# Performance work log

Hardware: AMD Instinct MI355X
Metric: run time of the kernel (lower is better)

The kernel has to match this reference:

```python
import jax, jax.numpy as jnp
import numpy as np

B, N = 1, 6
C, H, W = 256, 32, 88          # featureShape
ORH, ORW = 256, 704            # transformed image shape
OC = 128                       # out_channels
DV = jnp.arange(1.0, 45.0, 1.0)  # depth bin centers, d_conf=(1,45,1)
D = DV.shape[0]                # 44
BN_EPS = 1e-3


def _conv(x, w, b, pad):
    y = jax.lax.conv_general_dilated(x, w, (1, 1), [(pad, pad), (pad, pad)],
                                     dimension_numbers=("NCHW", "OIHW", "NCHW"))
    return y + b[None, :, None, None]


def _bn(x, g, be, m, v):
    scale = g / jnp.sqrt(v + BN_EPS)
    return (x - m[None, :, None, None]) * scale[None, :, None, None] + be[None, :, None, None]


def _frustum():
    ds = jnp.broadcast_to(DV[:, None, None], (D, H, W))
    xs = jnp.broadcast_to(jnp.linspace(0.0, ORW - 1.0, W)[None, None, :], (D, H, W))
    ys = jnp.broadcast_to(jnp.linspace(0.0, ORH - 1.0, H)[None, :, None], (D, H, W))
    return jnp.stack((xs, ys, ds), -1)  # (D,H,W,3)


def _forward(rot, trans, K, prot, ptrans, feats,
             w1, b1, g1, be1, m1, v1, w2, b2, g2, be2, m2, v2, w3, b3):
    # ---- geometry: undo image augmentation, unproject, map cam->ego ----
    fr = _frustum()
    pts = fr[None, None] - ptrans[:, :, None, None, None, :]              # (B,N,D,H,W,3)
    pts = jnp.einsum("bnij,bndhwj->bndhwi", jnp.linalg.inv(prot), pts)
    pts = jnp.concatenate((pts[..., :2] * pts[..., 2:3], pts[..., 2:3]), -1)
    combine = jnp.einsum("bnij,bnjk->bnik", rot, jnp.linalg.inv(K))
    geom = jnp.einsum("bnij,bndhwj->bndhwi", combine, pts) + trans[:, :, None, None, None, :]
    # ---- depth net (conv-bn-relu x2 + 1x1 head) ----
    x = feats.reshape(B * N, C, H, W)
    x = jax.nn.relu(_bn(_conv(x, w1, b1, 1), g1, be1, m1, v1))
    x = jax.nn.relu(_bn(_conv(x, w2, b2, 1), g2, be2, m2, v2))
    x = _conv(x, w3, b3, 0)                                              # (BN, OC+2, H, W)
    mu, log_sigma, f = x[:, 0], x[:, 1], x[:, 2:]
    sigma = jnp.exp(log_sigma) + 1e-6
    # per-pixel Gaussian over depth bins, normalized over D
    gauss = jnp.exp(-0.5 * (DV[None, :, None, None] - mu[:, None]) ** 2 / (sigma[:, None] ** 2))  # (BN,D,H,W)
    gauss = gauss / (gauss.sum(1, keepdims=True) + 1e-6)
    # outer product depth-dist x features -> (BN, OC, D, H, W)
    out = gauss[:, None] * f[:, :, None]
    out = out.reshape(B, N, OC, D, H, W).transpose(0, 1, 3, 4, 5, 2)     # (B,N,D,H,W,OC)
    return geom, out


def setup_inputs():
    key = jax.random.key(0)
    ks = jax.random.split(key, 9)
    eye = jnp.eye(3)
    rot = eye + 0.1 * jax.random.normal(ks[0], (B, N, 3, 3), jnp.float32)
    trans = jax.random.normal(ks[1], (B, N, 3), jnp.float32)
    Kbase = jnp.array([[600.0, 0.0, 352.0], [0.0, 600.0, 128.0], [0.0, 0.0, 1.0]])
    K = jnp.broadcast_to(Kbase, (B, N, 3, 3)) * (1.0 + 0.01 * jax.random.normal(ks[2], (B, N, 3, 3)))
    prot = eye + 0.05 * jax.random.normal(ks[3], (B, N, 3, 3), jnp.float32)
    ptrans = jax.random.normal(ks[4], (B, N, 3), jnp.float32)
    feats = 0.5 * jax.random.normal(ks[5], (B, N, C, H, W), jnp.float32)
    w1 = 0.02 * jax.random.normal(ks[6], (C, C, 3, 3), jnp.float32); b1 = jnp.zeros((C,))
    w2 = 0.02 * jax.random.normal(ks[7], (C, C, 3, 3), jnp.float32); b2 = jnp.zeros((C,))
    w3 = 0.02 * jax.random.normal(ks[8], (OC + 2, C, 1, 1), jnp.float32); b3 = jnp.zeros((OC + 2,))
    ones = jnp.ones((C,)); zeros = jnp.zeros((C,))
    return dict(cam2ego_rot=rot, cam2ego_trans=trans, cam_intrins=K,
                post_cam2ego_rot=prot, post_cam2ego_trans=ptrans, img_feats=feats,
                w1=w1, b1=b1, g1=ones, be1=zeros, m1=zeros, v1=ones,
                w2=w2, b2=b2, g2=ones, be2=zeros, m2=zeros, v2=ones,
                w3=w3, b3=b3)


def reference(cam2ego_rot, cam2ego_trans, cam_intrins, post_cam2ego_rot, post_cam2ego_trans, img_feats,
              w1, b1, g1, be1, m1, v1, w2, b2, g2, be2, m2, v2, w3, b3):
    return _forward(cam2ego_rot, cam2ego_trans, cam_intrins, post_cam2ego_rot, post_cam2ego_trans, img_feats,
                    w1, b1, g1, be1, m1, v1, w2, b2, g2, be2, m2, v2, w3, b3)
```

## Files before the change

kernel.cpp:

```cpp
#include <hip/hip_runtime.h>
#include <hip/hip_fp16.h>
#include <hip/hip_fp8.h>
#include <stdint.h>

typedef _Float16 f16;
typedef _Float16 half8 __attribute__((ext_vector_type(8)));
typedef _Float16 half4v __attribute__((ext_vector_type(4)));
typedef float floatx4 __attribute__((ext_vector_type(4)));
typedef long long i64;
typedef long long i64x2 __attribute__((ext_vector_type(2)));

#define NCAM 6
#define NPIX 16896
#define CIN 256
#define OUT1_OFF 2230272

#define AB_OFF     4096
#define W3P_OFF    16384
#define W1P_OFF    163840
#define W2P_OFF    1343488
#define XPAD_OFF   2523136
#define Y1P_OFF    11923456
#define XPAD8_BYTES 4700160
#define Y1P8_OFF   (XPAD_OFF + XPAD8_BYTES)
#define Y3_WS_OFF  21323776
#define Y3_BYTES   8921088

#define PIPE_BAR6()  asm volatile("s_waitcnt vmcnt(6) lgkmcnt(0)\n\ts_barrier" ::: "memory")
#define PIPE_BAR0()  asm volatile("s_waitcnt vmcnt(0) lgkmcnt(0)\n\ts_barrier" ::: "memory")
#define PIPE_BARL()  asm volatile("s_waitcnt lgkmcnt(0)\n\ts_barrier" ::: "memory")

__device__ __forceinline__ void gld16(const void* gsrc, void* ldst) {
    typedef __attribute__((address_space(1))) const uint32_t GBuf;
    typedef __attribute__((address_space(3))) uint32_t LBuf;
    __builtin_amdgcn_global_load_lds((GBuf*)(uintptr_t)gsrc,
                                     (LBuf*)(uint32_t)(uintptr_t)ldst,
                                     16, 0, 0);
}

__device__ __forceinline__ uint8_t f2fp8(float v) {
    __hip_fp8_e4m3 q(v);
    return (uint8_t)q.__x;
}

__device__ __forceinline__ int fp8pos(int c) {
    int c128 = c & 127;
    int P  = c128 >> 6;
    int kh = (c128 >> 5) & 1;
    int ks = (c128 >> 3) & 3;
    return (c >> 7) * 128 + (P * 4 + ks) * 16 + kh * 8 + (c & 7);
}

__device__ __forceinline__ void inv3(const float* m, float* o) {
    float a=m[0],b=m[1],c=m[2],d=m[3],e=m[4],f=m[5],g=m[6],h=m[7],i=m[8];
    float A  =  (e*i - f*h);
    float Bc = -(d*i - f*g);
    float Cc =  (d*h - e*g);
    float det = a*A + b*Bc + c*Cc;
    float r = 1.0f/det;
    o[0]=A*r;   o[1]=-(b*i - c*h)*r; o[2]= (b*f - c*e)*r;
    o[3]=Bc*r;  o[4]= (a*i - c*g)*r; o[5]=-(a*f - c*d)*r;
    o[6]=Cc*r;  o[7]=-(a*h - b*g)*r; o[8]= (a*e - b*d)*r;
}

__device__ __forceinline__ void geom_point(int idx,
        const float* __restrict__ rot, const float* __restrict__ trans,
        const float* __restrict__ K, const float* __restrict__ prot,
        const float* __restrict__ ptrans, float* __restrict__ out) {
    int w = idx % 88;
    int h = (idx / 88) % 32;
    int d = (idx / 2816) % 44;
    int n = idx / 123904;
    float P[9], Km[9], R[9], iP[9], iK[9], C[9];
    #pragma unroll
    for (int i = 0; i < 9; ++i) { P[i]=prot[n*9+i]; Km[i]=K[n*9+i]; R[i]=rot[n*9+i]; }
    inv3(P, iP);
    inv3(Km, iK);
    #pragma unroll
    for (int i = 0; i < 3; ++i)
        #pragma unroll
        for (int j = 0; j < 3; ++j)
            C[i*3+j] = R[i*3+0]*iK[0*3+j] + R[i*3+1]*iK[1*3+j] + R[i*3+2]*iK[2*3+j];
    float fx = w * (703.0f / 87.0f);
    float fy = h * (255.0f / 31.0f);
    float fz = d + 1.0f;
    float px = fx - ptrans[n*3+0], py = fy - ptrans[n*3+1], pz = fz - ptrans[n*3+2];
    float q0 = iP[0]*px + iP[1]*py + iP[2]*pz;
    float q1 = iP[3]*px + iP[4]*py + iP[5]*pz;
    float q2 = iP[6]*px + iP[7]*py + iP[8]*pz;
    float r0 = q0 * q2, r1 = q1 * q2, r2 = q2;
    out[idx*3 + 0] = C[0]*r0 + C[1]*r1 + C[2]*r2 + trans[n*3+0];
    out[idx*3 + 1] = C[3]*r0 + C[4]*r1 + C[5]*r2 + trans[n*3+1];
    out[idx*3 + 2] = C[6]*r0 + C[7]*r1 + C[8]*r2 + trans[n*3+2];
}

__global__ __launch_bounds__(256) void fused_prep(
        const float* __restrict__ rot, const float* __restrict__ trans,
        const float* __restrict__ K, const float* __restrict__ prot,
        const float* __restrict__ ptrans, const float* __restrict__ feats,
        const float* __restrict__ w1, const float* __restrict__ w2,
        const float* __restrict__ w3,
        const float* __restrict__ b1, const float* __restrict__ g1,
        const float* __restrict__ be1, const float* __restrict__ m1, const float* __restrict__ v1,
        const float* __restrict__ b2, const float* __restrict__ g2,
        const float* __restrict__ be2, const float* __restrict__ m2, const float* __restrict__ v2,
        const float* __restrict__ b3,
        uint8_t* __restrict__ w1p, uint8_t* __restrict__ w2p, f16* __restrict__ w3p,
        float* __restrict__ ab, uint8_t* __restrict__ xpad8, uint8_t* __restrict__ y1p8,
        float* __restrict__ geomOut) {
    int bid = blockIdx.x;
    int t = threadIdx.x;
    if (bid < 12) {
        uint8_t* buf = (bid < 6) ? xpad8 : y1p8;
        int n = bid % 6;
        for (int i = t; i < 3904; i += 256) {
            int u = i >> 4, c = i & 15;
            int h, w;
            if (u < 90)       { h = 0;       w = u; }
            else if (u < 180) { h = 33;      w = u - 90; }
            else if (u < 212) { h = u - 179; w = 0; }
            else              { h = u - 211; w = 89; }
            *(uint4*)&buf[((size_t)((n*34 + h)*90 + w))*256 + c*16] = uint4{0,0,0,0};
        }
        return;
    }
    if (bid < 716) {
        int oc = bid - 12;
        if (oc < 512) {
            const float* s = ((oc < 256) ? w1 : w2) + (size_t)(oc & 255) * 2304;
            uint8_t* dst = ((oc < 256) ? w1p : w2p) + (size_t)(oc & 255) * 2304;
            for (int idx = t; idx < 2304; idx += 256) {
                int win = idx >> 7, b = idx & 127;
                int sl = b >> 4, j = b & 15;
                int P = sl >> 2, ks = sl & 3, kh = j >> 3, jj = j & 7;
                int kwin = (2*P + kh)*32 + ks*8 + jj;
                int Kg = win*128 + kwin;
                int tap = Kg >> 8, c = Kg & 255;
                dst[idx] = f2fp8(s[c*9 + tap] * 16.0f);
            }
        } else {
            int r = oc - 512;
            w3p[r * 256 + t] = (r < 130) ? (f16)w3[r * 256 + t] : (f16)0.0f;
        }
        return;
    }
    if (bid < 1484) {
        __shared__ float tile[64][89];
        int b = bid - 716;
        int n = b >> 7;
        int h = (b >> 2) & 31;
        int icg = b & 3;
        int ic0 = icg * 64;
        #pragma unroll
        for (int j = 0; j < 22; ++j) {
            int idx = j * 256 + t;
            int r = idx / 88, w = idx - r * 88;
            tile[r][w] = feats[((size_t)(n*256 + ic0 + r) * 32 + h) * 88 + w];
        }
        __syncthreads();
        for (int j = 0; j < 6; ++j) {
            int idx = j * 256 + t;
            if (idx < 1408) {
                int w = idx >> 4, cq = idx & 15;
                int c = cq * 4;
                int ca = ic0 + c;
                uint32_t u = (uint32_t)f2fp8(tile[c][w])
                           | ((uint32_t)f2fp8(tile[c+1][w]) << 8)
                           | ((uint32_t)f2fp8(tile[c+2][w]) << 16)
                           | ((uint32_t)f2fp8(tile[c+3][w]) << 24);
                size_t px = (size_t)((n*34 + h + 1) * 90 + (w + 1));
                *(uint32_t*)&xpad8[px*256 + fp8pos(ca)] = u;
            }
        }
        return;
    }
    if (bid == 1484) {
        float a1 = g1[t] * rsqrtf(v1[t] + 1e-3f);
        ab[t]       = a1 * 0.0625f;
        ab[256 + t] = (b1[t] - m1[t]) * a1 + be1[t];
        float a2 = g2[t] * rsqrtf(v2[t] + 1e-3f);
        ab[512 + t] = a2 * 0.0625f;
        ab[768 + t] = (b2[t] - m2[t]) * a2 + be2[t];
        if (t < 192) ab[1024 + t] = (t < 130) ? b3[t] : 0.0f;
        return;
    }
    int idx = (bid - 1485) * 256 + t;
    geom_point(idx, rot, trans, K, prot, ptrans, geomOut);
}

__global__ void geom_k(const float* __restrict__ rot, const float* __restrict__ trans,
                       const float* __restrict__ K, const float* __restrict__ prot,
                       const float* __restrict__ ptrans, float* __restrict__ out) {
    int idx = blockIdx.x * 256 + threadIdx.x;
    geom_point(idx, rot, trans, K, prot, ptrans, out);
}

template<bool FP8OUT>
__global__ __launch_bounds__(256, 3) void conv8_mfma(
        const uint8_t* __restrict__ xin,
        const uint8_t* __restrict__ wp,
        const float* __restrict__ ab, int abOff,
        uint8_t* __restrict__ yout8,
        f16* __restrict__ yout16)
{
    __shared__ alignas(16) uint8_t Ald[2][64 * 128];
    __shared__ alignas(16) uint8_t Bld[2][128 * 128];
    int t = threadIdx.x;
    int l = t & 63;
    int wid = t >> 6;
    int bid = (blockIdx.x & 7) * 66 + (blockIdx.x >> 3);
    int bm = bid & 3;
    int bn = bid >> 2;
    int p0 = bn * 128;
    int wm = wid >> 1, wn = wid & 1;
    int swz = (l & 7) ^ (l >> 3);

    const uint8_t* asrc = wp + (size_t)(bm*64 + wid*16 + (l >> 3)) * 2304 + swz * 16;
    size_t bsrc[4];
    #pragma unroll
    for (int i = 0; i < 4; ++i) {
        int p = p0 + wid*32 + i*8 + (l >> 3);
        int n = p / 2816; int rem = p - n * 2816;
        int hh = rem / 88; int ww = rem - hh * 88;
        bsrc[i] = (size_t)((n*34 + hh) * 90 + ww) * 256 + swz * 16;
    }
    int aoff = wid * 2048 + l * 16;
    int boff = wid * 4096 + l * 16;

    floatx4 acc[2][4] = {};

    auto stage = [&](int win, uint8_t* Ab, uint8_t* Bb) {
        int tap = win >> 1;
        int koff = ((tap/3) * 90 + (tap%3)) * 256 + (win & 1) * 128;
        const uint8_t* aw = asrc + win * 128;
        gld16(aw,             Ab + aoff);
        gld16(aw + 8 * 2304,  Ab + aoff + 1024);
        #pragma unroll
        for (int j = 0; j < 4; ++j)
            gld16(xin + bsrc[j] + koff, Bb + boff + j * 1024);
    };
    auto compute = [&](const uint8_t* Ab, const uint8_t* Bb) {
        #pragma unroll
        for (int P = 0; P < 2; ++P) {
            i64x2 af[2], bf[4];
            int sl = (((P << 2) | (l >> 4)) ^ (l & 7)) * 16;
            #pragma unroll
            for (int m = 0; m < 2; ++m) {
                int row = wm*32 + m*16 + (l & 15);
                af[m] = *(const i64x2*)&Ab[row * 128 + sl];
            }
            #pragma unroll
            for (int n = 0; n < 4; ++n) {
                int row = wn*64 + n*16 + (l & 15);
                bf[n] = *(const i64x2*)&Bb[row * 128 + sl];
            }
            __builtin_amdgcn_s_setprio(1);
            #pragma unroll
            for (int m = 0; m < 2; ++m)
                #pragma unroll
                for (int n = 0; n < 4; ++n) {
                    acc[m][n] = __builtin_amdgcn_mfma_f32_16x16x32_fp8_fp8(af[m].x, bf[n].x, acc[m][n], 0, 0, 0);
                    acc[m][n] = __builtin_amdgcn_mfma_f32_16x16x32_fp8_fp8(af[m].y, bf[n].y, acc[m][n], 0, 0, 0);
                }
            __builtin_amdgcn_s_setprio(0);
        }
    };

    stage(0, Ald[0], Bld[0]);
    stage(1, Ald[1], Bld[1]);
    #pragma unroll 1
    for (int win = 0; win < 16; win += 2) {
        PIPE_BAR6(); compute(Ald[0], Bld[0]);
        PIPE_BARL(); stage(win + 2, Ald[0], Bld[0]);
        PIPE_BAR6(); compute(Ald[1], Bld[1]);
        PIPE_BARL(); stage(win + 3, Ald[1], Bld[1]);
    }
    PIPE_BAR6(); compute(Ald[0], Bld[0]);
    PIPE_BAR0(); compute(Ald[1], Bld[1]);

    int ocb = bm*64 + wm*32;
    #pragma unroll
    for (int m = 0; m < 2; ++m) {
        int oc0 = ocb + m*16 + (l >> 4) * 4;
        float4 av = *(const float4*)&ab[abOff + oc0];
        float4 bv = *(const float4*)&ab[abOff + 256 + oc0];
        #pragma unroll
        for (int n = 0; n < 4; ++n) {
            int p = p0 + wn*64 + n*16 + (l & 15);
            int ni = p / 2816; int rem = p - ni * 2816;
            int hh = rem / 88; int ww = rem - hh * 88;
            size_t pxb = (size_t)((ni*34 + hh + 1) * 90 + (ww + 1)) * 256;
            float v0 = fmaxf(fmaf(acc[m][n][0], av.x, bv.x), 0.0f);
            float v1 = fmaxf(fmaf(acc[m][n][1], av.y, bv.y), 0.0f);
            float v2 = fmaxf(fmaf(acc[m][n][2], av.z, bv.z), 0.0f);
            float v3 = fmaxf(fmaf(acc[m][n][3], av.w, bv.w), 0.0f);
            if (FP8OUT) {
                uint32_t u = (uint32_t)f2fp8(v0)
                           | ((uint32_t)f2fp8(v1) << 8)
                           | ((uint32_t)f2fp8(v2) << 16)
                           | ((uint32_t)f2fp8(v3) << 24);
                *(uint32_t*)&yout8[pxb + fp8pos(oc0)] = u;
            } else {
                half4v hv;
                hv[0] = (f16)v0; hv[1] = (f16)v1; hv[2] = (f16)v2; hv[3] = (f16)v3;
                *(half4v*)&yout16[pxb + oc0] = hv;
            }
        }
    }
}

__global__ __launch_bounds__(256) void conv3_mfma(
        const f16* __restrict__ xin,
        const f16* __restrict__ wp3,
        const float* __restrict__ b3p,
        float* __restrict__ y3)
{
    __shared__ alignas(16) f16 Ald[3][64 * 64];
    __shared__ alignas(16) f16 Bld[3][128 * 64];
    int t = threadIdx.x;
    int l = t & 63;
    int wid = t >> 6;
    int bm = blockIdx.x % 3;
    int bn = blockIdx.x / 3;
    int p0 = bn * 128;
    int wm = wid >> 1, wn = wid & 1;
    int swz = (l & 7) ^ (l >> 3);

    const f16* asrc = wp3 + (size_t)(bm*64 + wid*16 + (l >> 3)) * 256 + swz * 8;
    size_t bsrc[4];
    #pragma unroll
    for (int i = 0; i < 4; ++i) {
        int p = p0 + wid*32 + i*8 + (l >> 3);
        int n = p / 2816; int rem = p - n * 2816;
        int hh = rem / 88; int ww = rem - hh * 88;
        bsrc[i] = (size_t)((n*34 + hh) * 90 + ww) * 256 + swz * 8;
    }
    int aoff = wid * 16 * 64;
    int boff = wid * 32 * 64;

    floatx4 acc[2][4] = {};

    auto stage = [&](int kt, f16* Ab, f16* Bb) {
        int koff = (1 * 90 + 1) * 256 + kt * 64;
        int k0 = kt * 64;
        gld16(asrc + k0,            Ab + aoff);
        gld16(asrc + k0 + 8 * 256,  Ab + aoff + 8 * 64);
        gld16(xin + bsrc[0] + koff, Bb + boff);
        gld16(xin + bsrc[1] + koff, Bb + boff + 8 * 64);
        gld16(xin + bsrc[2] + koff, Bb + boff + 16 * 64);
        gld16(xin + bsrc[3] + koff, Bb + boff + 24 * 64);
    };
    auto compute = [&](const f16* Ab, const f16* Bb) {
        #pragma unroll
        for (int kk = 0; kk < 2; ++kk) {
            half8 af[2], bf[4];
            int kslot = kk * 4 + (l >> 4);
            #pragma unroll
            for (int m = 0; m < 2; ++m) {
                int row = wm*32 + m*16 + (l & 15);
                af[m] = *(const half8*)&Ab[row * 64 + ((kslot ^ (row & 7)) * 8)];
            }
            #pragma unroll
            for (int n = 0; n < 4; ++n) {
                int row = wn*64 + n*16 + (l & 15);
                bf[n] = *(const half8*)&Bb[row * 64 + ((kslot ^ (row & 7)) * 8)];
            }
            __builtin_amdgcn_s_setprio(1);
            #pragma unroll
            for (int m = 0; m < 2; ++m)
                #pragma unroll
                for (int n = 0; n < 4; ++n)
                    acc[m][n] = __builtin_amdgcn_mfma_f32_16x16x32_f16(af[m], bf[n], acc[m][n], 0, 0, 0);
            __builtin_amdgcn_s_setprio(0);
        }
    };

    stage(0, Ald[0], Bld[0]);
    stage(1, Ald[1], Bld[1]);
    PIPE_BAR6(); stage(2, Ald[2], Bld[2]); compute(Ald[0], Bld[0]);
    PIPE_BAR6(); stage(3, Ald[0], Bld[0]); compute(Ald[1], Bld[1]);
    PIPE_BAR6(); compute(Ald[2], Bld[2]);
    PIPE_BAR0(); compute(Ald[0], Bld[0]);

    int ocb = bm*64 + wm*32;
    #pragma unroll
    for (int m = 0; m < 2; ++m) {
        int oc0 = ocb + m*16 + (l >> 4) * 4;
        if (oc0 < 132) {
            float4 bv = *(const float4*)&b3p[oc0];
            #pragma unroll
            for (int n = 0; n < 4; ++n) {
                int p = p0 + wn*64 + n*16 + (l & 15);
                float4 v;
                v.x = acc[m][n][0] + bv.x;
                v.y = acc[m][n][1] + bv.y;
                v.z = acc[m][n][2] + bv.z;
                v.w = acc[m][n][3] + bv.w;
                *(float4*)&y3[(size_t)p * 132 + oc0] = v;
            }
        }
    }
}

__global__ __launch_bounds__(256) void splat_k(
        const float* __restrict__ y3,
        float* __restrict__ out)
{
    __shared__ float eg[8][44];
    __shared__ float rs[8];
    int t = threadIdx.x;
    int p0 = blockIdx.x * 8;

    for (int i = t; i < 352; i += 256) {
        int px = i / 44, d = i - px * 44;
        const float* row = y3 + (size_t)(p0 + px) * 132;
        float mu = row[0];
        float sig = expf(row[1]) + 1e-6f;
        float z = (d + 1.0f) - mu;
        eg[px][d] = expf(-0.5f * z * z / (sig * sig));
    }
    __syncthreads();
    if (t < 8) {
        float s = 0.0f;
        for (int d = 0; d < 44; ++d) s += eg[t][d];
        rs[t] = 1.0f / (s + 1e-6f);
    }
    __syncthreads();

    int l = t & 63;
    int wid = t >> 6;
    int px = wid * 2 + (l >> 5);
    int ch = (l & 31) * 4;
    int p = p0 + px;
    int n = p / 2816; int rem = p - n * 2816;
    int h = rem / 88; int w = rem - h * 88;
    const float* row = y3 + (size_t)p * 132;
    floatx4 f4 = *(const floatx4*)&row[2 + ch];
    float rsv = rs[px];

    size_t pxb = ((size_t)(n * 44) * 32 + h) * 88 + w;
    float* o1 = out + OUT1_OFF;
    #pragma unroll 4
    for (int d = 0; d < 44; ++d) {
        float gg = eg[px][d] * rsv;
        floatx4 v;
        v.x = gg * f4.x; v.y = gg * f4.y; v.z = gg * f4.z; v.w = gg * f4.w;
        __builtin_nontemporal_store(v, (floatx4*)&o1[(pxb + (size_t)d * 2816) * 128 + ch]);
    }
}

extern "C" void kernel_launch(void* const* d_in, const int* in_sizes, int n_in,
                              void* d_out, int out_size, void* d_ws, size_t ws_size,
                              hipStream_t stream) {
    const float* rot    = (const float*)d_in[0];
    const float* trans  = (const float*)d_in[1];
    const float* K      = (const float*)d_in[2];
    const float* prot   = (const float*)d_in[3];
    const float* ptrans = (const float*)d_in[4];
    const float* feats  = (const float*)d_in[5];
    const float* w1     = (const float*)d_in[6];
    const float* b1     = (const float*)d_in[7];
    const float* g1     = (const float*)d_in[8];
    const float* be1    = (const float*)d_in[9];
    const float* m1     = (const float*)d_in[10];
    const float* v1     = (const float*)d_in[11];
    const float* w2     = (const float*)d_in[12];
    const float* b2     = (const float*)d_in[13];
    const float* g2     = (const float*)d_in[14];
    const float* be2    = (const float*)d_in[15];
    const float* m2     = (const float*)d_in[16];
    const float* v2     = (const float*)d_in[17];
    const float* w3     = (const float*)d_in[18];
    const float* b3     = (const float*)d_in[19];

    char* ws = (char*)d_ws;
    float*   ab    = (float*)(ws + AB_OFF);
    f16*     w3p   = (f16*)(ws + W3P_OFF);
    uint8_t* w1p8  = (uint8_t*)(ws + W1P_OFF);
    uint8_t* w2p8  = (uint8_t*)(ws + W2P_OFF);
    uint8_t* xpad8 = (uint8_t*)(ws + XPAD_OFF);
    uint8_t* y1p8  = (uint8_t*)(ws + Y1P8_OFF);
    f16*     y2    = (f16*)(ws + Y1P_OFF);
    float*   out   = (float*)d_out;

    bool y3InWs = ws_size >= (size_t)(Y3_WS_OFF + Y3_BYTES);
    float* y3 = y3InWs ? (float*)(ws + Y3_WS_OFF) : out;
    int geomBlocks = y3InWs ? 2904 : 0;

    fused_prep<<<1485 + geomBlocks, 256, 0, stream>>>(
        rot, trans, K, prot, ptrans, feats, w1, w2, w3,
        b1, g1, be1, m1, v1, b2, g2, be2, m2, v2, b3,
        w1p8, w2p8, w3p, ab, xpad8, y1p8, out);
    conv8_mfma<true><<<528, 256, 0, stream>>>(xpad8, w1p8, ab, 0, y1p8, nullptr);
    conv8_mfma<false><<<528, 256, 0, stream>>>(y1p8, w2p8, ab, 512, nullptr, y2);
    conv3_mfma<<<396, 256, 0, stream>>>(y2, w3p, ab + 1024, y3);
    splat_k<<<2112, 256, 0, stream>>>(y3, out);
    if (!y3InWs)
        geom_k<<<2904, 256, 0, stream>>>(rot, trans, K, prot, ptrans, out);
}
```

Baseline: 131.8 us.

## Fuse 1x1 head conv into splat kernel and move geometry blocks there

Removes the separate MFMA 1x1 head convolution and its fp32 y3 intermediate. Each splat block now loads its 8 pixels' fp16 features into LDS and computes the 130 head outputs with scalar FMAs before doing the Gaussian depth splat. Geometry computation moves from the prep kernel into extra blocks of the splat kernel. This cuts one launch and the y3 global round trip, but replaces tensor-core matmul with per-thread scalar FMAs where only 130 of 256 threads work, and each block rereads the full head weights.

```diff
diff --git a/kernel.cpp b/kernel.cpp
--- a/kernel.cpp
+++ b/kernel.cpp
@@ -23,8 +23,6 @@
 #define Y1P_OFF    11923456
 #define XPAD8_BYTES 4700160
 #define Y1P8_OFF   (XPAD_OFF + XPAD8_BYTES)
-#define Y3_WS_OFF  21323776
-#define Y3_BYTES   8921088
 
 #define PIPE_BAR6()  asm volatile("s_waitcnt vmcnt(6) lgkmcnt(0)\n\ts_barrier" ::: "memory")
 #define PIPE_BAR0()  asm volatile("s_waitcnt vmcnt(0) lgkmcnt(0)\n\ts_barrier" ::: "memory")
@@ -95,9 +93,7 @@
 }
 
 __global__ __launch_bounds__(256) void fused_prep(
-        const float* __restrict__ rot, const float* __restrict__ trans,
-        const float* __restrict__ K, const float* __restrict__ prot,
-        const float* __restrict__ ptrans, const float* __restrict__ feats,
+        const float* __restrict__ feats,
         const float* __restrict__ w1, const float* __restrict__ w2,
         const float* __restrict__ w3,
         const float* __restrict__ b1, const float* __restrict__ g1,
@@ -106,8 +102,7 @@
         const float* __restrict__ be2, const float* __restrict__ m2, const float* __restrict__ v2,
         const float* __restrict__ b3,
         uint8_t* __restrict__ w1p, uint8_t* __restrict__ w2p, f16* __restrict__ w3p,
-        float* __restrict__ ab, uint8_t* __restrict__ xpad8, uint8_t* __restrict__ y1p8,
-        float* __restrict__ geomOut) {
+        float* __restrict__ ab, uint8_t* __restrict__ xpad8, uint8_t* __restrict__ y1p8) {
     int bid = blockIdx.x;
     int t = threadIdx.x;
     if (bid < 12) {
@@ -174,7 +169,7 @@
         }
         return;
     }
-    if (bid == 1484) {
+    {
         float a1 = g1[t] * rsqrtf(v1[t] + 1e-3f);
         ab[t]       = a1 * 0.0625f;
         ab[256 + t] = (b1[t] - m1[t]) * a1 + be1[t];
@@ -182,17 +177,7 @@
         ab[512 + t] = a2 * 0.0625f;
         ab[768 + t] = (b2[t] - m2[t]) * a2 + be2[t];
         if (t < 192) ab[1024 + t] = (t < 130) ? b3[t] : 0.0f;
-        return;
-    }
-    int idx = (bid - 1485) * 256 + t;
-    geom_point(idx, rot, trans, K, prot, ptrans, geomOut);
-}
-
-__global__ void geom_k(const float* __restrict__ rot, const float* __restrict__ trans,
-                       const float* __restrict__ K, const float* __restrict__ prot,
-                       const float* __restrict__ ptrans, float* __restrict__ out) {
-    int idx = blockIdx.x * 256 + threadIdx.x;
-    geom_point(idx, rot, trans, K, prot, ptrans, out);
+    }
 }
 
 template<bool FP8OUT>
@@ -309,114 +294,71 @@
     }
 }
 
-__global__ __launch_bounds__(256) void conv3_mfma(
-        const f16* __restrict__ xin,
+__global__ __launch_bounds__(256) void splat_fused(
+        const f16* __restrict__ y2,
         const f16* __restrict__ wp3,
         const float* __restrict__ b3p,
-        float* __restrict__ y3)
-{
-    __shared__ alignas(16) f16 Ald[3][64 * 64];
-    __shared__ alignas(16) f16 Bld[3][128 * 64];
-    int t = threadIdx.x;
-    int l = t & 63;
-    int wid = t >> 6;
-    int bm = blockIdx.x % 3;
-    int bn = blockIdx.x / 3;
-    int p0 = bn * 128;
-    int wm = wid >> 1, wn = wid & 1;
-    int swz = (l & 7) ^ (l >> 3);
-
-    const f16* asrc = wp3 + (size_t)(bm*64 + wid*16 + (l >> 3)) * 256 + swz * 8;
-    size_t bsrc[4];
-    #pragma unroll
-    for (int i = 0; i < 4; ++i) {
-        int p = p0 + wid*32 + i*8 + (l >> 3);
-        int n = p / 2816; int rem = p - n * 2816;
-        int hh = rem / 88; int ww = rem - hh * 88;
-        bsrc[i] = (size_t)((n*34 + hh) * 90 + ww) * 256 + swz * 8;
-    }
-    int aoff = wid * 16 * 64;
-    int boff = wid * 32 * 64;
-
-    floatx4 acc[2][4] = {};
-
-    auto stage = [&](int kt, f16* Ab, f16* Bb) {
-        int koff = (1 * 90 + 1) * 256 + kt * 64;
-        int k0 = kt * 64;
-        gld16(asrc + k0,            Ab + aoff);
-        gld16(asrc + k0 + 8 * 256,  Ab + aoff + 8 * 64);
-        gld16(xin + bsrc[0] + koff, Bb + boff);
-        gld16(xin + bsrc[1] + koff, Bb + boff + 8 * 64);
-        gld16(xin + bsrc[2] + koff, Bb + boff + 16 * 64);
-        gld16(xin + bsrc[3] + koff, Bb + boff + 24 * 64);
-    };
-    auto compute = [&](const f16* Ab, const f16* Bb) {
-        #pragma unroll
-        for (int kk = 0; kk < 2; ++kk) {
-            half8 af[2], bf[4];
-            int kslot = kk * 4 + (l >> 4);
-            #pragma unroll
-            for (int m = 0; m < 2; ++m) {
-                int row = wm*32 + m*16 + (l & 15);
-                af[m] = *(const half8*)&Ab[row * 64 + ((kslot ^ (row & 7)) * 8)];
-            }
-            #pragma unroll
-            for (int n = 0; n < 4; ++n) {
-                int row = wn*64 + n*16 + (l & 15);
-                bf[n] = *(const half8*)&Bb[row * 64 + ((kslot ^ (row & 7)) * 8)];
-            }
-            __builtin_amdgcn_s_setprio(1);
-            #pragma unroll
-            for (int m = 0; m < 2; ++m)
-                #pragma unroll
-                for (int n = 0; n < 4; ++n)
-                    acc[m][n] = __builtin_amdgcn_mfma_f32_16x16x32_f16(af[m], bf[n], acc[m][n], 0, 0, 0);
-            __builtin_amdgcn_s_setprio(0);
-        }
-    };
-
-    stage(0, Ald[0], Bld[0]);
-    stage(1, Ald[1], Bld[1]);
-    PIPE_BAR6(); stage(2, Ald[2], Bld[2]); compute(Ald[0], Bld[0]);
-    PIPE_BAR6(); stage(3, Ald[0], Bld[0]); compute(Ald[1], Bld[1]);
-    PIPE_BAR6(); compute(Ald[2], Bld[2]);
-    PIPE_BAR0(); compute(Ald[0], Bld[0]);
-
-    int ocb = bm*64 + wm*32;
-    #pragma unroll
-    for (int m = 0; m < 2; ++m) {
-        int oc0 = ocb + m*16 + (l >> 4) * 4;
-        if (oc0 < 132) {
-            float4 bv = *(const float4*)&b3p[oc0];
-            #pragma unroll
-            for (int n = 0; n < 4; ++n) {
-                int p = p0 + wn*64 + n*16 + (l & 15);
-                float4 v;
-                v.x = acc[m][n][0] + bv.x;
-                v.y = acc[m][n][1] + bv.y;
-                v.z = acc[m][n][2] + bv.z;
-                v.w = acc[m][n][3] + bv.w;
-                *(float4*)&y3[(size_t)p * 132 + oc0] = v;
-            }
-        }
-    }
-}
-
-__global__ __launch_bounds__(256) void splat_k(
-        const float* __restrict__ y3,
+        const float* __restrict__ rot, const float* __restrict__ trans,
+        const float* __restrict__ K, const float* __restrict__ prot,
+        const float* __restrict__ ptrans,
         float* __restrict__ out)
 {
+    int t = threadIdx.x;
+    int bid = blockIdx.x;
+    if (bid >= 2112) {
+        int idx = (bid - 2112) * 256 + t;
+        geom_point(idx, rot, trans, K, prot, ptrans, out);
+        return;
+    }
+
+    __shared__ alignas(16) f16 y2l[8 * 256];
+    __shared__ alignas(16) float fl[8][128];
+    __shared__ float muA[8], lsA[8], rs[8];
     __shared__ float eg[8][44];
-    __shared__ float rs[8];
-    int t = threadIdx.x;
-    int p0 = blockIdx.x * 8;
+
+    int p0 = bid * 8;
+    {
+        int px = t >> 5, c = t & 31;
+        int p = p0 + px;
+        int n = p / 2816; int rem = p - n * 2816;
+        int h = rem / 88; int w = rem - h * 88;
+        const f16* src = y2 + (size_t)((n*34 + h + 1) * 90 + (w + 1)) * 256 + c * 8;
+        gld16(src, (uint8_t*)y2l + t * 16);
+    }
+    PIPE_BAR0();
+
+    if (t < 130) {
+        float acc[8] = {};
+        const f16* wrow = wp3 + (size_t)t * 256;
+        #pragma unroll 4
+        for (int c = 0; c < 32; ++c) {
+            half8 wv = *(const half8*)&wrow[c * 8];
+            #pragma unroll
+            for (int px = 0; px < 8; ++px) {
+                half8 yv = *(const half8*)&y2l[px * 256 + c * 8];
+                #pragma unroll
+                for (int j = 0; j < 8; ++j)
+                    acc[px] = fmaf((float)wv[j], (float)yv[j], acc[px]);
+            }
+        }
+        float bias = b3p[t];
+        if (t == 0) {
+            #pragma unroll
+            for (int px = 0; px < 8; ++px) muA[px] = acc[px] + bias;
+        } else if (t == 1) {
+            #pragma unroll
+            for (int px = 0; px < 8; ++px) lsA[px] = acc[px] + bias;
+        } else {
+            #pragma unroll
+            for (int px = 0; px < 8; ++px) fl[px][t - 2] = acc[px] + bias;
+        }
+    }
+    __syncthreads();
 
     for (int i = t; i < 352; i += 256) {
         int px = i / 44, d = i - px * 44;
-        const float* row = y3 + (size_t)(p0 + px) * 132;
-        float mu = row[0];
-        float sig = expf(row[1]) + 1e-6f;
-        float z = (d + 1.0f) - mu;
+        float sig = expf(lsA[px]) + 1e-6f;
+        float z = (d + 1.0f) - muA[px];
         eg[px][d] = expf(-0.5f * z * z / (sig * sig));
     }
     __syncthreads();
@@ -434,8 +376,7 @@
     int p = p0 + px;
     int n = p / 2816; int rem = p - n * 2816;
     int h = rem / 88; int w = rem - h * 88;
-    const float* row = y3 + (size_t)p * 132;
-    floatx4 f4 = *(const floatx4*)&row[2 + ch];
+    floatx4 f4 = *(const floatx4*)&fl[px][ch];
     float rsv = rs[px];
 
     size_t pxb = ((size_t)(n * 44) * 32 + h) * 88 + w;
@@ -483,18 +424,12 @@
     f16*     y2    = (f16*)(ws + Y1P_OFF);
     float*   out   = (float*)d_out;
 
-    bool y3InWs = ws_size >= (size_t)(Y3_WS_OFF + Y3_BYTES);
-    float* y3 = y3InWs ? (float*)(ws + Y3_WS_OFF) : out;
-    int geomBlocks = y3InWs ? 2904 : 0;
-
-    fused_prep<<<1485 + geomBlocks, 256, 0, stream>>>(
-        rot, trans, K, prot, ptrans, feats, w1, w2, w3,
+    fused_prep<<<1485, 256, 0, stream>>>(
+        feats, w1, w2, w3,
         b1, g1, be1, m1, v1, b2, g2, be2, m2, v2, b3,
-        w1p8, w2p8, w3p, ab, xpad8, y1p8, out);
+        w1p8, w2p8, w3p, ab, xpad8, y1p8);
     conv8_mfma<true><<<528, 256, 0, stream>>>(xpad8, w1p8, ab, 0, y1p8, nullptr);
     conv8_mfma<false><<<528, 256, 0, stream>>>(y1p8, w2p8, ab, 512, nullptr, y2);
-    conv3_mfma<<<396, 256, 0, stream>>>(y2, w3p, ab + 1024, y3);
-    splat_k<<<2112, 256, 0, stream>>>(y3, out);
-    if (!y3InWs)
-        geom_k<<<2904, 256, 0, stream>>>(rot, trans, K, prot, ptrans, out);
-}
+    splat_fused<<<5016, 256, 0, stream>>>(y2, w3p, ab + 1024,
+                                          rot, trans, K, prot, ptrans, out);
+}
```

Measured after the change: 150.6 us. 1.14x slower.
